# Kernel optimization log

Measured on AMD Instinct MI355X. Metric: run time of the kernel, lower is better.

Reference implementation:

```python
import jax, jax.numpy as jnp
import numpy as np

N, E, F, HID, HEADS, L, OUT = 25000, 400000, 128, 128, 2, 3, 10
C = HID // HEADS
EPS = 1e-5

def _ln(x, g, b):
    m = jnp.mean(x, -1, keepdims=True)
    v = jnp.mean((x - m) ** 2, -1, keepdims=True)
    return (x - m) / jnp.sqrt(v + EPS) * g + b

def _lrelu(x, s=0.01):
    return jnp.where(x >= 0, x, s * x)

def setup_inputs():
    key = jax.random.key(0)
    ks = iter(jax.random.split(key, 80))
    def nrm(shape, fan_in):
        return jax.random.normal(next(ks), shape, dtype=jnp.float32) / np.float32(np.sqrt(fan_in))
    return {
        "x": jax.random.normal(next(ks), (N, F), dtype=jnp.float32),
        "edge_index": jax.random.randint(next(ks), (2, E), 0, N, dtype=jnp.int32),
        "edge_attr": jax.random.uniform(next(ks), (E,), dtype=jnp.float32),
        "task_features": jax.random.normal(next(ks), (4,), dtype=jnp.float32),
        "emb_w": nrm((F, HID), F), "emb_b": jnp.zeros((HID,), jnp.float32),
        "emb_g": jnp.ones((HID,), jnp.float32), "emb_beta": jnp.zeros((HID,), jnp.float32),
        "gat_w": nrm((L, HID, HID), HID),
        "gat_as": nrm((L, HEADS, C), C), "gat_ad": nrm((L, HEADS, C), C),
        "gat_bias": jnp.zeros((L, HID), jnp.float32),
        "ec_w1": nrm((L, 2 * HID, HID), 2 * HID), "ec_b1": jnp.zeros((L, HID), jnp.float32),
        "ec_g1": jnp.ones((L, HID), jnp.float32), "ec_be1": jnp.zeros((L, HID), jnp.float32),
        "ec_w2": nrm((L, HID, HID), HID), "ec_b2": jnp.zeros((L, HID), jnp.float32),
        "ec_g2": jnp.ones((L, HID), jnp.float32), "ec_be2": jnp.zeros((L, HID), jnp.float32),
        "norm_g": jnp.ones((L, HID), jnp.float32), "norm_b": jnp.zeros((L, HID), jnp.float32),
        "task_w": nrm((4, HID), 4), "task_b": jnp.zeros((HID,), jnp.float32),
        "task_g": jnp.ones((HID,), jnp.float32), "task_beta": jnp.zeros((HID,), jnp.float32),
        "pa_w1": nrm((HID, HID // 2), HID), "pa_b1": jnp.zeros((HID // 2,), jnp.float32),
        "pa_w2": nrm((HID // 2, 1), HID // 2), "pa_b2": jnp.zeros((1,), jnp.float32),
        "v_w1": nrm((2 * HID, HID), 2 * HID), "v_b1": jnp.zeros((HID,), jnp.float32),
        "v_g": jnp.ones((HID,), jnp.float32), "v_be": jnp.zeros((HID,), jnp.float32),
        "v_w2": nrm((HID, 1), HID), "v_b2": jnp.zeros((1,), jnp.float32),
        "a_w1": nrm((2 * HID, HID), 2 * HID), "a_b1": jnp.zeros((HID,), jnp.float32),
        "a_g": jnp.ones((HID,), jnp.float32), "a_be": jnp.zeros((HID,), jnp.float32),
        "a_w2": nrm((HID, OUT), HID), "a_b2": jnp.zeros((OUT,), jnp.float32),
    }

def _forward(x, edge_attr, task_features, emb_w, emb_b, emb_g, emb_beta,
             gat_w, gat_as, gat_ad, gat_bias,
             ec_w1, ec_b1, ec_g1, ec_be1, ec_w2, ec_b2, ec_g2, ec_be2,
             norm_g, norm_b, task_w, task_b, task_g, task_beta,
             pa_w1, pa_b1, pa_w2, pa_b2,
             v_w1, v_b1, v_g, v_be, v_w2, v_b2,
             a_w1, a_b1, a_g, a_be, a_w2, a_b2, edge_index):
    src, dst = edge_index[0], edge_index[1]
    loop = jnp.arange(N, dtype=edge_index.dtype)
    src_sl = jnp.concatenate([src, loop])  # PyG GATConv adds self-loops
    dst_sl = jnp.concatenate([dst, loop])
    h = _lrelu(_ln(x @ emb_w + emb_b, emb_g, emb_beta))
    x0 = h
    for i in range(L):
        # --- GATConv (dropout inactive at eval) ---
        ht = (h @ gat_w[i]).reshape(N, HEADS, C)
        a_s = jnp.sum(ht * gat_as[i], -1)  # [N, HEADS]
        a_d = jnp.sum(ht * gat_ad[i], -1)
        e = _lrelu(a_s[src_sl] + a_d[dst_sl], 0.2)  # [E+N, HEADS]
        emax = jax.ops.segment_max(e, dst_sl, num_segments=N)
        ee = jnp.exp(e - emax[dst_sl])
        alpha = ee / jax.ops.segment_sum(ee, dst_sl, num_segments=N)[dst_sl]
        x1 = jax.ops.segment_sum(ht[src_sl] * alpha[:, :, None], dst_sl,
                                 num_segments=N).reshape(N, HID) + gat_bias[i]
        # --- EdgeConv: gather -> MLP -> weighted scatter-add ---
        ef = jnp.concatenate([h[src], h[dst]], axis=1)  # [E, 2*HID]
        ef = _lrelu(_ln(ef @ ec_w1[i] + ec_b1[i], ec_g1[i], ec_be1[i]), 0.2)
        ef = _lrelu(_ln(ef @ ec_w2[i] + ec_b2[i], ec_g2[i], ec_be2[i]), 0.2)
        ef = ef * edge_attr[:, None]
        x2 = jax.ops.segment_sum(ef, dst, num_segments=N)
        h = _lrelu(_ln(x1 + x2, norm_g[i], norm_b[i]))
        if i > 0:
            h = h + x0
            x0 = h
    # attention pooling over all nodes (batch=None path)
    w = jax.nn.softmax((_lrelu(h @ pa_w1 + pa_b1) @ pa_w2 + pa_b2)[:, 0])
    gf = jnp.sum(h * w[:, None], axis=0)  # [HID]
    te = _lrelu(_ln(task_features @ task_w + task_b, task_g, task_beta))
    cf = jnp.concatenate([gf, te], -1)  # [2*HID]
    value = _lrelu(_ln(cf @ v_w1 + v_b1, v_g, v_be)) @ v_w2 + v_b2
    adv = _lrelu(_ln(cf @ a_w1 + a_b1, a_g, a_be)) @ a_w2 + a_b2
    return value + (adv - jnp.mean(adv, -1, keepdims=True))

def reference(x, edge_index, edge_attr, task_features, emb_w, emb_b, emb_g, emb_beta, gat_w, gat_as, gat_ad, gat_bias, ec_w1, ec_b1, ec_g1, ec_be1, ec_w2, ec_b2, ec_g2, ec_be2, norm_g, norm_b, task_w, task_b, task_g, task_beta, pa_w1, pa_b1, pa_w2, pa_b2, v_w1, v_b1, v_g, v_be, v_w2, v_b2, a_w1, a_b1, a_g, a_be, a_w2, a_b2):
    return _forward(x, edge_attr, task_features, emb_w, emb_b, emb_g, emb_beta, gat_w, gat_as, gat_ad, gat_bias, ec_w1, ec_b1, ec_g1, ec_be1, ec_w2, ec_b2, ec_g2, ec_be2, norm_g, norm_b, task_w, task_b, task_g, task_beta, pa_w1, pa_b1, pa_w2, pa_b2, v_w1, v_b1, v_g, v_be, v_w2, v_b2, a_w1, a_b1, a_g, a_be, a_w2, a_b2, edge_index)
```

## Files before the change

kernel.cpp:

```cpp
#include <hip/hip_runtime.h>
#include <math.h>

#define NN 25000
#define EE 400000
#define LL 3
#define LNEPS 1e-5f
#define EB 64

typedef __attribute__((ext_vector_type(8))) short short8;
typedef __attribute__((ext_vector_type(16))) float f32x16;

__device__ __forceinline__ float lrelu(float x, float s) { return fmaxf(x, x * s); }

__device__ __forceinline__ unsigned int pack_bf2(float lo, float hi) {
    unsigned int ul = __float_as_uint(lo), uh = __float_as_uint(hi);
    ul = (ul + 0x7FFFu + ((ul >> 16) & 1u)) >> 16;
    uh = (uh + 0x7FFFu + ((uh >> 16) & 1u)) >> 16;
    return (uh << 16) | (ul & 0xFFFFu);
}

__device__ __forceinline__ void ln_stats128(float v, float* red, float& mean, float& inv) {
    float sm = v, sq = v * v;
#pragma unroll
    for (int m = 32; m >= 1; m >>= 1) { sm += __shfl_xor(sm, m); sq += __shfl_xor(sq, m); }
    __syncthreads();
    if ((threadIdx.x & 63) == 0) { red[(threadIdx.x >> 6) * 2] = sm; red[(threadIdx.x >> 6) * 2 + 1] = sq; }
    __syncthreads();
    sm = red[0] + red[2]; sq = red[1] + red[3];
    mean = sm * (1.f / 128.f);
    float var = sq * (1.f / 128.f) - mean * mean;
    inv = rsqrtf(var + LNEPS);
}

__global__ void k_hist(const int* __restrict__ dst, int* __restrict__ cnt, int ne)
{
    int i = blockIdx.x * 256 + threadIdx.x;
    if (i < ne) atomicAdd(&cnt[dst[i]], 1);
}

__global__ __launch_bounds__(1024) void k_scan(const int* __restrict__ cnt,
                                               int* __restrict__ starts, int n)
{
    __shared__ int tot[1024];
    int t = threadIdx.x;
    const int PER = (n + 1023) >> 10;
    int i0 = t * PER;
    int s = 0;
    for (int k = 0; k < PER; ++k) { int i = i0 + k; s += (i < n) ? cnt[i] : 0; }
    tot[t] = s;
    __syncthreads();
    for (int off = 1; off < 1024; off <<= 1) {
        int x = (t >= off) ? tot[t - off] : 0;
        __syncthreads();
        tot[t] += x;
        __syncthreads();
    }
    int run = (t > 0) ? tot[t - 1] : 0;
    for (int k = 0; k < PER; ++k) {
        int i = i0 + k;
        if (i < n) { starts[i] = run; run += cnt[i]; }
    }
    if (t == 1023) starts[n] = tot[1023];
}

__global__ void k_scatter(const int* __restrict__ src, const int* __restrict__ dst,
                          const float* __restrict__ ea, int* __restrict__ cursor,
                          int* __restrict__ s_src, int* __restrict__ s_dst,
                          float* __restrict__ s_ea, int ne)
{
    int i = blockIdx.x * 256 + threadIdx.x;
    if (i >= ne) return;
    int d = dst[i];
    int pos = atomicAdd(&cursor[d], 1);
    s_src[pos] = src[i];
    s_dst[pos] = d;
    s_ea[pos] = ea[i];
}

__global__ void k_prep(const float* __restrict__ gat_w, const float* __restrict__ ec_w1,
                       const float* __restrict__ ec_w2, const float* __restrict__ emb_w,
                       uint4* __restrict__ wf)
{
    int g = blockIdx.x * 256 + threadIdx.x;
    int m = g >> 11, f = g & 2047;
    const float* srcm;
    if (m < 3) srcm = gat_w + (size_t)m * 16384;
    else if (m < 9) { int t2 = m - 3; srcm = ec_w1 + (size_t)(t2 >> 1) * 32768 + (size_t)(t2 & 1) * 16384; }
    else if (m < 12) srcm = ec_w2 + (size_t)(m - 9) * 16384;
    else srcm = emb_w;
    int l = f & 63, ks = (f >> 6) & 7, nb = f >> 9;
    int k0 = ks * 16 + (l >> 5) * 8, col = nb * 32 + (l & 31);
    const float* wp = srcm + (size_t)k0 * 128 + col;
    uint4 r;
    r.x = pack_bf2(wp[0],   wp[128]);
    r.y = pack_bf2(wp[256], wp[384]);
    r.z = pack_bf2(wp[512], wp[640]);
    r.w = pack_bf2(wp[768], wp[896]);
    wf[g] = r;
}

__global__ __launch_bounds__(256) void k_emb(
    const float* __restrict__ in, const uint4* __restrict__ wfm,
    const float* __restrict__ bias, const float* __restrict__ g,
    const float* __restrict__ be, float* __restrict__ h,
    float* __restrict__ x0, int nrows)
{
    __shared__ __align__(16) unsigned int sA[64 * 64];
    __shared__ __align__(16) unsigned int sW[2048 * 4];
    float* sU = (float*)sW;
    const int tid = threadIdx.x;
    const int r0 = blockIdx.x * 64;
    {
        int row = tid >> 2, q = tid & 3;
        const float* srcp = in + (size_t)(r0 + row) * 128 + q * 32;
        bool ok = (r0 + row) < nrows;
#pragma unroll
        for (int i = 0; i < 8; ++i) {
            float4 v = ok ? *(const float4*)&srcp[i * 4] : make_float4(0.f, 0.f, 0.f, 0.f);
            int cu = (q * 16 + i * 2) ^ ((row & 15) << 2);
            *(uint2*)&sA[row * 64 + cu] = make_uint2(pack_bf2(v.x, v.y), pack_bf2(v.z, v.w));
        }
    }
    {
        uint4* sW4 = (uint4*)sW;
#pragma unroll
        for (int i = 0; i < 8; ++i) sW4[tid + 256 * i] = wfm[tid + 256 * i];
    }
    __syncthreads();
    const int w = tid >> 6, l = tid & 63;
    const int m0 = (w >> 1) * 32, nhalf = (w & 1);
    f32x16 acc0 = {}, acc1 = {};
#pragma unroll
    for (int ks = 0; ks < 8; ++ks) {
        int rw = m0 + (l & 31);
        int cu = (ks * 8 + (l >> 5) * 4) ^ ((rw & 15) << 2);
        short8 a = *(const short8*)&sA[rw * 64 + cu];
        short8 b0 = *(const short8*)&sW[((nhalf * 16 + ks) * 64 + l) * 4];
        short8 b1 = *(const short8*)&sW[(((nhalf * 2 + 1) * 8 + ks) * 64 + l) * 4];
        acc0 = __builtin_amdgcn_mfma_f32_32x32x16_bf16(a, b0, acc0, 0, 0, 0);
        acc1 = __builtin_amdgcn_mfma_f32_32x32x16_bf16(a, b1, acc1, 0, 0, 0);
    }
    __syncthreads();
    {
        int colbase = nhalf * 64 + (l & 31);
        float bb0 = bias[colbase], bb1 = bias[colbase + 32];
#pragma unroll
        for (int r = 0; r < 16; ++r) {
            int rw = m0 + (r & 3) + 8 * (r >> 2) + 4 * (l >> 5);
            sU[rw * 128 + colbase]      = acc0[r] + bb0;
            sU[rw * 128 + colbase + 32] = acc1[r] + bb1;
        }
    }
    __syncthreads();
    float2 gv = *(const float2*)&g[l * 2];
    float2 bv = *(const float2*)&be[l * 2];
    for (int it = 0; it < 16; ++it) {
        int rw = w * 16 + it;
        int grow = r0 + rw;
        if (grow >= nrows) break;
        float2 v = *(const float2*)&sU[rw * 128 + l * 2];
        float sm = v.x + v.y, sq = v.x * v.x + v.y * v.y;
#pragma unroll
        for (int m = 32; m >= 1; m >>= 1) { sm += __shfl_xor(sm, m); sq += __shfl_xor(sq, m); }
        float mean = sm * (1.f / 128.f);
        float var = sq * (1.f / 128.f) - mean * mean;
        float inv = rsqrtf(var + LNEPS);
        float o0 = lrelu((v.x - mean) * inv * gv.x + bv.x, 0.01f);
        float o1 = lrelu((v.y - mean) * inv * gv.y + bv.y, 0.01f);
        unsigned off = (unsigned)grow * 128u + (unsigned)(l * 2);
        *(float2*)&h[off]  = make_float2(o0, o1);
        *(float2*)&x0[off] = make_float2(o0, o1);
    }
}

__global__ __launch_bounds__(256) void k_gemm3(
    const float* __restrict__ in, const uint4* __restrict__ wf,
    int mht, int mA, int mB, const float* __restrict__ bA,
    float* __restrict__ o0, float* __restrict__ o1, float* __restrict__ o2,
    int nrows)
{
    __shared__ __align__(16) unsigned int sA[64 * 64];
    __shared__ __align__(16) unsigned int sW[2048 * 4];
    const int tid = threadIdx.x;
    const int r0 = blockIdx.x * 64;
    {
        int row = tid >> 2, q = tid & 3;
        const float* srcp = in + (size_t)(r0 + row) * 128 + q * 32;
        bool ok = (r0 + row) < nrows;
#pragma unroll
        for (int i = 0; i < 8; ++i) {
            float4 v = ok ? *(const float4*)&srcp[i * 4] : make_float4(0.f, 0.f, 0.f, 0.f);
            unsigned int p0 = pack_bf2(v.x, v.y), p1 = pack_bf2(v.z, v.w);
            int cu = (q * 16 + i * 2) ^ ((row & 15) << 2);
            *(uint2*)&sA[row * 64 + cu] = make_uint2(p0, p1);
        }
    }
    __syncthreads();
    const int w = tid >> 6, l = tid & 63;
    const int m0 = (w >> 1) * 32, nhalf = (w & 1);
    short8 af[8];
#pragma unroll
    for (int ks = 0; ks < 8; ++ks) {
        int row = m0 + (l & 31);
        int cu = (ks * 8 + (l >> 5) * 4) ^ ((row & 15) << 2);
        af[ks] = *(const short8*)&sA[row * 64 + cu];
    }
    auto do_mat = [&](int mat, float* out, const float* bp) {
        __syncthreads();
        {
            const uint4* wsrc = wf + (size_t)mat * 2048;
            uint4* sW4 = (uint4*)sW;
#pragma unroll
            for (int i = 0; i < 8; ++i) sW4[tid + 256 * i] = wsrc[tid + 256 * i];
        }
        __syncthreads();
        f32x16 acc0 = {}, acc1 = {};
        const int nb0 = nhalf * 2;
#pragma unroll
        for (int ks = 0; ks < 8; ++ks) {
            short8 b0 = *(const short8*)&sW[((nb0 * 8 + ks) * 64 + l) * 4];
            short8 b1v = *(const short8*)&sW[(((nb0 + 1) * 8 + ks) * 64 + l) * 4];
            acc0 = __builtin_amdgcn_mfma_f32_32x32x16_bf16(af[ks], b0, acc0, 0, 0, 0);
            acc1 = __builtin_amdgcn_mfma_f32_32x32x16_bf16(af[ks], b1v, acc1, 0, 0, 0);
        }
        int colbase = nhalf * 64 + (l & 31);
        float badd0 = bp ? bp[colbase] : 0.f;
        float badd1 = bp ? bp[colbase + 32] : 0.f;
#pragma unroll
        for (int r = 0; r < 16; ++r) {
            int row = r0 + m0 + (r & 3) + 8 * (r >> 2) + 4 * (l >> 5);
            if (row < nrows) {
                unsigned off = (unsigned)row * 128u + (unsigned)colbase;
                out[off]      = acc0[r] + badd0;
                out[off + 32] = acc1[r] + badd1;
            }
        }
    };
    do_mat(mht, o0, nullptr);
    do_mat(mA, o1, bA);
    do_mat(mB, o2, nullptr);
}

__global__ __launch_bounds__(512) void k_node_scores(
    const float* __restrict__ ht, const float* __restrict__ A, const float* __restrict__ B,
    const float* __restrict__ as_, const float* __restrict__ ad_,
    float* __restrict__ a_s, float* __restrict__ a_d,
    float* __restrict__ denom, float* __restrict__ selfe,
    float* __restrict__ rsA, float* __restrict__ rsB, int n)
{
    int wv = threadIdx.x >> 6, ln = threadIdx.x & 63;
    int node = blockIdx.x * 8 + wv;
    if (node >= n) return;
    unsigned off = (unsigned)node * 128u + (unsigned)(ln * 2);
    float2 hv = *(const float2*)&ht[off];
    float2 av = *(const float2*)&A[off];
    float2 bv = *(const float2*)&B[off];
    float2 wsv = *(const float2*)&as_[ln * 2];
    float2 wdv = *(const float2*)&ad_[ln * 2];
    float ss = hv.x * wsv.x + hv.y * wsv.y;
    float sd = hv.x * wdv.x + hv.y * wdv.y;
    float sa = av.x + av.y, sb = bv.x + bv.y;
#pragma unroll
    for (int m = 16; m >= 1; m >>= 1) {
        ss += __shfl_xor(ss, m); sd += __shfl_xor(sd, m);
        sa += __shfl_xor(sa, m); sb += __shfl_xor(sb, m);
    }
    float sa2 = sa + __shfl_xor(sa, 32);
    float sb2 = sb + __shfl_xor(sb, 32);
    if ((ln & 31) == 0) {
        int hd = ln >> 5;
        a_s[node * 2 + hd] = ss;
        a_d[node * 2 + hd] = sd;
        float ev = expf(lrelu(ss + sd, 0.2f));
        denom[node * 2 + hd] = ev;
        selfe[node * 2 + hd] = ev;
        if (hd == 0) { rsA[node] = sa2; rsB[node] = sb2; }
    }
}

__global__ void k_edge_denom2(const int* __restrict__ s_src, const int* __restrict__ s_dst,
                              const float* __restrict__ a_s, const float* __restrict__ a_d,
                              float* __restrict__ denom, int ne)
{
    int base = (blockIdx.x * 256 + threadIdx.x) * 8;
    if (base >= ne) return;
    int curd = -1;
    float acc0 = 0.f, acc1 = 0.f;
    for (int k = 0; k < 8; ++k) {
        int e = base + k;
        if (e >= ne) break;
        int s = s_src[e], d = s_dst[e];
        float v0 = expf(lrelu(a_s[(unsigned)(s * 2)]     + a_d[(unsigned)(d * 2)],     0.2f));
        float v1 = expf(lrelu(a_s[(unsigned)(s * 2 + 1)] + a_d[(unsigned)(d * 2 + 1)], 0.2f));
        if (d != curd) {
            if (curd >= 0) { atomicAdd(&denom[curd * 2], acc0); atomicAdd(&denom[curd * 2 + 1], acc1); }
            curd = d; acc0 = v0; acc1 = v1;
        } else { acc0 += v0; acc1 += v1; }
    }
    if (curd >= 0) { atomicAdd(&denom[curd * 2], acc0); atomicAdd(&denom[curd * 2 + 1], acc1); }
}

__global__ void k_xsum_init(const float* __restrict__ ht, const float* __restrict__ selfe,
                            const float* __restrict__ denom,
                            const float* __restrict__ gbias, float* __restrict__ xsum, int n)
{
    unsigned idx = blockIdx.x * blockDim.x + threadIdx.x;
    if (idx >= (unsigned)n * 128u) return;
    unsigned node = idx >> 7, c = idx & 127, hd = c >> 6;
    float alpha = selfe[node * 2 + hd] / denom[node * 2 + hd];
    xsum[idx] = gbias[c] + ht[idx] * alpha;
}

__global__ __launch_bounds__(512) void k_edge_main(
    const float* __restrict__ Abuf, const float* __restrict__ Bbuf,
    const float* __restrict__ ht,
    const int* __restrict__ s_src, const int* __restrict__ s_dst,
    const float* __restrict__ s_ea,
    const float* __restrict__ a_s, const float* __restrict__ a_d,
    const float* __restrict__ denom,
    const uint4* __restrict__ w2f,
    const float* __restrict__ rsA, const float* __restrict__ rsB,
    const float* __restrict__ g1, const float* __restrict__ be1,
    const float* __restrict__ b2, const float* __restrict__ g2, const float* __restrict__ be2,
    float* __restrict__ xsum, int ne)
{
    __shared__ __align__(16) unsigned int sWB[2048 * 4];
    __shared__ __align__(16) unsigned int sT32[EB * 64];
    __shared__ int   sS[EB], sD[EB];
    __shared__ float sEA[EB], sM[EB];
    __shared__ float sAl[EB * 2];
    __shared__ float sG1[128], sE1[128], sB2[128], sG2[128], sE2[128];
    float* sU = (float*)sWB;

    const int tid = threadIdx.x;
    {
        uint4* sWB4 = (uint4*)sWB;
#pragma unroll
        for (int i = 0; i < 4; ++i) { int f = tid + 512 * i; sWB4[f] = w2f[f]; }
    }
    if (tid < 128) {
        sG1[tid] = g1[tid]; sE1[tid] = be1[tid];
        sB2[tid] = b2[tid]; sG2[tid] = g2[tid]; sE2[tid] = be2[tid];
    }
    const int e0 = blockIdx.x * EB;
    const int nev = (ne - e0 < EB) ? (ne - e0) : EB;
    if (tid < EB) {
        if (tid < nev) {
            int s = s_src[e0 + tid], d = s_dst[e0 + tid];
            sS[tid] = s; sD[tid] = d; sEA[tid] = s_ea[e0 + tid];
            sM[tid] = (rsA[s] + rsB[d]) * (1.f / 128.f);
        } else { sS[tid] = 0; sD[tid] = -1; sEA[tid] = 0.f; sM[tid] = 0.f; }
    }
    if (tid < 2 * EB) {
        int le = tid >> 1, hd = tid & 1;
        float al = 0.f;
        if (le < nev) {
            int e = e0 + le;
            int s = s_src[e], d = s_dst[e];
            float ev = lrelu(a_s[(unsigned)(s * 2 + hd)] + a_d[(unsigned)(d * 2 + hd)], 0.2f);
            al = expf(ev) / denom[(unsigned)(d * 2 + hd)];
        }
        sAl[le * 2 + hd] = al;
    }
    __syncthreads();

    const int wv = tid >> 6, ln = tid & 63;
    const unsigned ln2 = (unsigned)(ln * 2);
    {
        const float g1a = sG1[ln * 2], g1b = sG1[ln * 2 + 1];
        const float e1a = sE1[ln * 2], e1b = sE1[ln * 2 + 1];
        for (int j = 0; j < 8; ++j) {
            int e = wv * 8 + j;
            if (e < nev) {
                unsigned s = (unsigned)sS[e], d = (unsigned)sD[e];
                float mean = sM[e];
                float2 av = *(const float2*)&Abuf[s * 128u + ln2];
                float2 bv = *(const float2*)&Bbuf[d * 128u + ln2];
                float v0 = av.x + bv.x - mean;
                float v1 = av.y + bv.y - mean;
                float sq = v0 * v0 + v1 * v1;
#pragma unroll
                for (int m = 32; m >= 1; m >>= 1) sq += __shfl_xor(sq, m);
                float inv = rsqrtf(sq * (1.f / 128.f) + LNEPS);
                float t0 = lrelu(v0 * inv * g1a + e1a, 0.2f);
                float t1 = lrelu(v1 * inv * g1b + e1b, 0.2f);
                sT32[e * 64 + (ln ^ ((e & 15) << 2))] = pack_bf2(t0, t1);
            }
        }
    }
    __syncthreads();

    {
        const int w = wv, l = ln;
        const int m0 = (w >> 2) * 32, n0 = (w & 3) * 32;
        f32x16 acc = {};
#pragma unroll
        for (int ks = 0; ks < 8; ++ks) {
            int row = m0 + (l & 31);
            int colu = (ks * 8 + (l >> 5) * 4) ^ ((row & 15) << 2);
            short8 a = *(const short8*)&sT32[row * 64 + colu];
            short8 b = *(const short8*)&sWB[((((w & 3) * 8 + ks) * 64 + l)) * 4];
            acc = __builtin_amdgcn_mfma_f32_32x32x16_bf16(a, b, acc, 0, 0, 0);
        }
        __syncthreads();
        float b2c = sB2[n0 + (l & 31)];
#pragma unroll
        for (int r = 0; r < 16; ++r) {
            int row = m0 + (r & 3) + 8 * (r >> 2) + 4 * (l >> 5);
            sU[row * 128 + n0 + (l & 31)] = acc[r] + b2c;
        }
    }
    __syncthreads();

    {
        const float g2a = sG2[ln * 2], g2b = sG2[ln * 2 + 1];
        const float e2a = sE2[ln * 2], e2b = sE2[ln * 2 + 1];
        int curd = -1;
        float acc0 = 0.f, acc1 = 0.f;
        for (int j = 0; j < 8; ++j) {
            int e = wv * 8 + j;
            if (e >= nev) break;
            unsigned s = (unsigned)sS[e];
            int d = sD[e];
            float2 uv = *(const float2*)&sU[e * 128 + ln * 2];
            float u0 = uv.x, u1 = uv.y;
            float sm = u0 + u1, sq = u0 * u0 + u1 * u1;
#pragma unroll
            for (int m = 32; m >= 1; m >>= 1) { sm += __shfl_xor(sm, m); sq += __shfl_xor(sq, m); }
            float mean = sm * (1.f / 128.f);
            float var = sq * (1.f / 128.f) - mean * mean;
            float inv = rsqrtf(var + LNEPS);
            float eav = sEA[e];
            float v0 = lrelu((u0 - mean) * inv * g2a + e2a, 0.2f) * eav;
            float v1 = lrelu((u1 - mean) * inv * g2b + e2b, 0.2f) * eav;
            float al = sAl[e * 2 + (ln >> 5)];
            float2 hv = *(const float2*)&ht[s * 128u + ln2];
            v0 += hv.x * al;
            v1 += hv.y * al;
            if (d != curd) {
                if (curd >= 0) {
                    atomicAdd(&xsum[(unsigned)curd * 128u + ln2], acc0);
                    atomicAdd(&xsum[(unsigned)curd * 128u + ln2 + 1], acc1);
                }
                curd = d; acc0 = v0; acc1 = v1;
            } else { acc0 += v0; acc1 += v1; }
        }
        if (curd >= 0) {
            atomicAdd(&xsum[(unsigned)curd * 128u + ln2], acc0);
            atomicAdd(&xsum[(unsigned)curd * 128u + ln2 + 1], acc1);
        }
    }
}

__global__ __launch_bounds__(512) void k_norm8(const float* __restrict__ xsum,
                                               const float* __restrict__ g,
                                               const float* __restrict__ b,
                                               float* __restrict__ x0,
                                               float* __restrict__ h, int n, int layer)
{
    int wv = threadIdx.x >> 6, ln = threadIdx.x & 63;
    int node = blockIdx.x * 8 + wv;
    if (node >= n) return;
    unsigned off = (unsigned)node * 128u + (unsigned)(ln * 2);
    float2 v = *(const float2*)&xsum[off];
    float sm = v.x + v.y, sq = v.x * v.x + v.y * v.y;
#pragma unroll
    for (int m = 32; m >= 1; m >>= 1) { sm += __shfl_xor(sm, m); sq += __shfl_xor(sq, m); }
    float mean = sm * (1.f / 128.f);
    float var = sq * (1.f / 128.f) - mean * mean;
    float inv = rsqrtf(var + LNEPS);
    float2 gv = *(const float2*)&g[ln * 2];
    float2 bv = *(const float2*)&b[ln * 2];
    float val0 = lrelu((v.x - mean) * inv * gv.x + bv.x, 0.01f);
    float val1 = lrelu((v.y - mean) * inv * gv.y + bv.y, 0.01f);
    if (layer > 0) {
        float2 x0v = *(const float2*)&x0[off];
        val0 += x0v.x; val1 += x0v.y;
        *(float2*)&x0[off] = make_float2(val0, val1);
    }
    *(float2*)&h[off] = make_float2(val0, val1);
}

__global__ __launch_bounds__(256) void k_pool_score(const float* __restrict__ h,
    const float* __restrict__ w1, const float* __restrict__ b1,
    const float* __restrict__ w2, const float* __restrict__ b2,
    float* __restrict__ score, int n)
{
    int wv = threadIdx.x >> 6, ln = threadIdx.x & 63;
    int node = blockIdx.x * 4 + wv;
    if (node >= n) return;
    float acc = b1[ln];
    const float* hr = h + (size_t)node * 128;
    for (int k = 0; k < 128; ++k) acc += hr[k] * w1[k * 64 + ln];
    acc = lrelu(acc, 0.01f) * w2[ln];
#pragma unroll
    for (int m = 32; m >= 1; m >>= 1) acc += __shfl_xor(acc, m);
    if (ln == 0) score[node] = acc + b2[0];
}

__global__ __launch_bounds__(256) void k_softmax_reduce(const float* __restrict__ score,
                                                        float* __restrict__ stats,
                                                        float* __restrict__ gf, int n)
{
    __shared__ float red[8];
    int t = threadIdx.x;
    float mx = -1e30f;
    for (int i = t; i < n; i += 256) mx = fmaxf(mx, score[i]);
#pragma unroll
    for (int m = 32; m >= 1; m >>= 1) mx = fmaxf(mx, __shfl_xor(mx, m));
    if ((t & 63) == 0) red[t >> 6] = mx;
    __syncthreads();
    mx = fmaxf(fmaxf(red[0], red[1]), fmaxf(red[2], red[3]));
    float s = 0.f;
    for (int i = t; i < n; i += 256) s += expf(score[i] - mx);
#pragma unroll
    for (int m = 32; m >= 1; m >>= 1) s += __shfl_xor(s, m);
    if ((t & 63) == 0) red[4 + (t >> 6)] = s;
    __syncthreads();
    s = red[4] + red[5] + red[6] + red[7];
    if (t == 0) { stats[0] = mx; stats[1] = s; }
    if (t < 128) gf[t] = 0.f;
}

__global__ __launch_bounds__(128) void k_gf(const float* __restrict__ h,
                                            const float* __restrict__ score,
                                            const float* __restrict__ stats,
                                            float* __restrict__ gf, int n)
{
    int c = threadIdx.x;
    float mx = stats[0], invZ = 1.f / stats[1];
    int per = (n + gridDim.x - 1) / gridDim.x;
    int n0 = blockIdx.x * per;
    int n1 = n0 + per; if (n1 > n) n1 = n;
    float acc = 0.f;
    for (int i = n0; i < n1; ++i)
        acc += expf(score[i] - mx) * invZ * h[(size_t)i * 128 + c];
    atomicAdd(&gf[c], acc);
}

__global__ __launch_bounds__(128) void k_head(
    const float* __restrict__ gf, const float* __restrict__ tf,
    const float* __restrict__ task_w, const float* __restrict__ task_b,
    const float* __restrict__ task_g, const float* __restrict__ task_be,
    const float* __restrict__ v_w1, const float* __restrict__ v_b1,
    const float* __restrict__ v_g, const float* __restrict__ v_be,
    const float* __restrict__ v_w2, const float* __restrict__ v_b2,
    const float* __restrict__ a_w1, const float* __restrict__ a_b1,
    const float* __restrict__ a_g, const float* __restrict__ a_be,
    const float* __restrict__ a_w2, const float* __restrict__ a_b2,
    float* __restrict__ out)
{
    __shared__ float cf[256], hbuf[128], red[4], sc[2], adv[10];
    int t = threadIdx.x;
    float mean, inv;
    float te = task_b[t];
#pragma unroll
    for (int k = 0; k < 4; ++k) te += tf[k] * task_w[k * 128 + t];
    ln_stats128(te, red, mean, inv);
    te = lrelu((te - mean) * inv * task_g[t] + task_be[t], 0.01f);
    cf[t] = gf[t]; cf[128 + t] = te;
    __syncthreads();
    float v = v_b1[t];
    for (int k = 0; k < 256; ++k) v += cf[k] * v_w1[k * 128 + t];
    ln_stats128(v, red, mean, inv);
    v = lrelu((v - mean) * inv * v_g[t] + v_be[t], 0.01f);
    float pv = v * v_w2[t];
#pragma unroll
    for (int m = 32; m >= 1; m >>= 1) pv += __shfl_xor(pv, m);
    __syncthreads();
    if ((t & 63) == 0) red[t >> 6] = pv;
    __syncthreads();
    if (t == 0) sc[0] = red[0] + red[1] + v_b2[0];
    float a = a_b1[t];
    for (int k = 0; k < 256; ++k) a += cf[k] * a_w1[k * 128 + t];
    ln_stats128(a, red, mean, inv);
    a = lrelu((a - mean) * inv * a_g[t] + a_be[t], 0.01f);
    hbuf[t] = a;
    __syncthreads();
    if (t < 10) {
        float s = a_b2[t];
        for (int c = 0; c < 128; ++c) s += hbuf[c] * a_w2[c * 10 + t];
        adv[t] = s;
    }
    __syncthreads();
    if (t == 0) {
        float m10 = 0.f;
        for (int o = 0; o < 10; ++o) m10 += adv[o];
        sc[1] = m10 * 0.1f;
    }
    __syncthreads();
    if (t < 10) out[t] = sc[0] + adv[t] - sc[1];
}

extern "C" void kernel_launch(void* const* d_in, const int* in_sizes, int n_in,
                              void* d_out, int out_size, void* d_ws, size_t ws_size,
                              hipStream_t stream)
{
    const float* x        = (const float*)d_in[0];
    const int*   ei       = (const int*)d_in[1];
    const float* ea       = (const float*)d_in[2];
    const float* tf       = (const float*)d_in[3];
    const float* emb_w    = (const float*)d_in[4];
    const float* emb_b    = (const float*)d_in[5];
    const float* emb_g    = (const float*)d_in[6];
    const float* emb_beta = (const float*)d_in[7];
    const float* gat_w    = (const float*)d_in[8];
    const float* gat_as   = (const float*)d_in[9];
    const float* gat_ad   = (const float*)d_in[10];
    const float* gat_bias = (const float*)d_in[11];
    const float* ec_w1    = (const float*)d_in[12];
    const float* ec_b1    = (const float*)d_in[13];
    const float* ec_g1    = (const float*)d_in[14];
    const float* ec_be1   = (const float*)d_in[15];
    const float* ec_w2    = (const float*)d_in[16];
    const float* ec_b2    = (const float*)d_in[17];
    const float* ec_g2    = (const float*)d_in[18];
    const float* ec_be2   = (const float*)d_in[19];
    const float* norm_g   = (const float*)d_in[20];
    const float* norm_b   = (const float*)d_in[21];
    const float* task_w   = (const float*)d_in[22];
    const float* task_b   = (const float*)d_in[23];
    const float* task_g   = (const float*)d_in[24];
    const float* task_be  = (const float*)d_in[25];
    const float* pa_w1    = (const float*)d_in[26];
    const float* pa_b1    = (const float*)d_in[27];
    const float* pa_w2    = (const float*)d_in[28];
    const float* pa_b2    = (const float*)d_in[29];
    const float* v_w1     = (const float*)d_in[30];
    const float* v_b1     = (const float*)d_in[31];
    const float* v_g      = (const float*)d_in[32];
    const float* v_be     = (const float*)d_in[33];
    const float* v_w2     = (const float*)d_in[34];
    const float* v_b2     = (const float*)d_in[35];
    const float* a_w1     = (const float*)d_in[36];
    const float* a_b1     = (const float*)d_in[37];
    const float* a_g      = (const float*)d_in[38];
    const float* a_be     = (const float*)d_in[39];
    const float* a_w2     = (const float*)d_in[40];
    const float* a_b2     = (const float*)d_in[41];

    const int n = in_sizes[0] / 128;
    const int e = in_sizes[2];
    const int* src = ei;
    const int* dst = ei + e;

    float* ws = (float*)d_ws;
    uint4* wf = (uint4*)ws;
    float* base = ws + 13 * 2048 * 4;
    const size_t NR = (size_t)n * 128;
    float* h    = base;
    float* x0   = base + NR;
    float* ht   = base + 2 * NR;
    float* A    = base + 3 * NR;
    float* B    = base + 4 * NR;
    float* xs   = base + 5 * NR;
    float* a_s  = base + 6 * NR;
    float* a_d  = a_s + (size_t)n * 2;
    float* den  = a_d + (size_t)n * 2;
    float* selfe = den + (size_t)n * 2;
    float* rsA  = selfe + (size_t)n * 2;
    float* rsB  = rsA + n;
    float* score = rsB + n;
    float* stats = score + n;
    float* gf    = stats + 2;
    int*   cnt    = (int*)(gf + 128);
    int*   starts = cnt + n;
    int*   s_src  = starts + (n + 1);
    int*   s_dst  = s_src + e;
    float* s_ea   = (float*)(s_dst + e);

    const int ng64 = (n + 63) / 64;
    const int ng8 = (n + 7) / 8;

    hipMemsetAsync(cnt, 0, (size_t)n * sizeof(int), stream);
    k_hist<<<(e + 255) / 256, 256, 0, stream>>>(dst, cnt, e);
    k_scan<<<1, 1024, 0, stream>>>(cnt, starts, n);
    hipMemcpyAsync(cnt, starts, (size_t)n * sizeof(int), hipMemcpyDeviceToDevice, stream);
    k_scatter<<<(e + 255) / 256, 256, 0, stream>>>(src, dst, ea, cnt, s_src, s_dst, s_ea, e);
    k_prep<<<104, 256, 0, stream>>>(gat_w, ec_w1, ec_w2, emb_w, wf);

    k_emb<<<ng64, 256, 0, stream>>>(x, wf + (size_t)12 * 2048, emb_b, emb_g, emb_beta, h, x0, n);

    for (int i = 0; i < LL; ++i) {
        k_gemm3<<<ng64, 256, 0, stream>>>(h, wf, i, 3 + 2 * i, 4 + 2 * i,
                                          ec_b1 + i * 128, ht, A, B, n);
        k_node_scores<<<ng8, 512, 0, stream>>>(ht, A, B, gat_as + i * 128, gat_ad + i * 128,
                                               a_s, a_d, den, selfe, rsA, rsB, n);
        k_edge_denom2<<<((e + 7) / 8 + 255) / 256, 256, 0, stream>>>(s_src, s_dst, a_s, a_d, den, e);
        k_xsum_init<<<(n * 128 + 255) / 256, 256, 0, stream>>>(ht, selfe, den,
                                                               gat_bias + i * 128, xs, n);
        k_edge_main<<<(e + EB - 1) / EB, 512, 0, stream>>>(A, B, ht, s_src, s_dst, s_ea,
                                                           a_s, a_d, den,
                                                           wf + (size_t)(9 + i) * 2048,
                                                           rsA, rsB,
                                                           ec_g1 + i * 128, ec_be1 + i * 128,
                                                           ec_b2 + i * 128, ec_g2 + i * 128, ec_be2 + i * 128,
                                                           xs, e);
        k_norm8<<<ng8, 512, 0, stream>>>(xs, norm_g + i * 128, norm_b + i * 128, x0, h, n, i);
    }

    k_pool_score<<<(n + 3) / 4, 256, 0, stream>>>(h, pa_w1, pa_b1, pa_w2, pa_b2, score, n);
    k_softmax_reduce<<<1, 256, 0, stream>>>(score, stats, gf, n);
    k_gf<<<200, 128, 0, stream>>>(h, score, stats, gf, n);
    k_head<<<1, 128, 0, stream>>>(gf, tf, task_w, task_b, task_g, task_be,
                                  v_w1, v_b1, v_g, v_be, v_w2, v_b2,
                                  a_w1, a_b1, a_g, a_be, a_w2, a_b2,
                                  (float*)d_out);
}
```

Before: 803.5 us.

## Store GEMM outputs ht, A, B as packed bf16 to halve gather traffic

```diff
diff --git a/kernel.cpp b/kernel.cpp
--- a/kernel.cpp
+++ b/kernel.cpp
@@ -18,6 +18,8 @@
     uh = (uh + 0x7FFFu + ((uh >> 16) & 1u)) >> 16;
     return (uh << 16) | (ul & 0xFFFFu);
 }
+__device__ __forceinline__ float bf_lo(unsigned int u) { return __uint_as_float(u << 16); }
+__device__ __forceinline__ float bf_hi(unsigned int u) { return __uint_as_float(u & 0xFFFF0000u); }
 
 __device__ __forceinline__ void ln_stats128(float v, float* red, float& mean, float& inv) {
     float sm = v, sq = v * v;
@@ -176,7 +178,7 @@
 __global__ __launch_bounds__(256) void k_gemm3(
     const float* __restrict__ in, const uint4* __restrict__ wf,
     int mht, int mA, int mB, const float* __restrict__ bA,
-    float* __restrict__ o0, float* __restrict__ o1, float* __restrict__ o2,
+    unsigned* __restrict__ o0, unsigned* __restrict__ o1, unsigned* __restrict__ o2,
     int nrows)
 {
     __shared__ __align__(16) unsigned int sA[64 * 64];
@@ -205,7 +207,10 @@
         int cu = (ks * 8 + (l >> 5) * 4) ^ ((row & 15) << 2);
         af[ks] = *(const short8*)&sA[row * 64 + cu];
     }
-    auto do_mat = [&](int mat, float* out, const float* bp) {
+    const int c = l & 31;
+    const bool evenl = (c & 1) == 0;
+    const unsigned uidx = (unsigned)(nhalf * 32 + (evenl ? (c >> 1) : (16 + (c >> 1))));
+    auto do_mat = [&](int mat, unsigned* out, const float* bp) {
         __syncthreads();
         {
             const uint4* wsrc = wf + (size_t)mat * 2048;
@@ -223,16 +228,19 @@
             acc0 = __builtin_amdgcn_mfma_f32_32x32x16_bf16(af[ks], b0, acc0, 0, 0, 0);
             acc1 = __builtin_amdgcn_mfma_f32_32x32x16_bf16(af[ks], b1v, acc1, 0, 0, 0);
         }
-        int colbase = nhalf * 64 + (l & 31);
+        int colbase = nhalf * 64 + c;
         float badd0 = bp ? bp[colbase] : 0.f;
         float badd1 = bp ? bp[colbase + 32] : 0.f;
 #pragma unroll
         for (int r = 0; r < 16; ++r) {
+            float v0 = acc0[r] + badd0;
+            float v1 = acc1[r] + badd1;
+            float v0p = __shfl_xor(v0, 1);
+            float v1p = __shfl_xor(v1, 1);
             int row = r0 + m0 + (r & 3) + 8 * (r >> 2) + 4 * (l >> 5);
             if (row < nrows) {
-                unsigned off = (unsigned)row * 128u + (unsigned)colbase;
-                out[off]      = acc0[r] + badd0;
-                out[off + 32] = acc1[r] + badd1;
+                unsigned val = evenl ? pack_bf2(v0, v0p) : pack_bf2(v1p, v1);
+                out[(unsigned)row * 64u + uidx] = val;
             }
         }
     };
@@ -242,7 +250,8 @@
 }
 
 __global__ __launch_bounds__(512) void k_node_scores(
-    const float* __restrict__ ht, const float* __restrict__ A, const float* __restrict__ B,
+    const unsigned* __restrict__ htp, const unsigned* __restrict__ Apk,
+    const unsigned* __restrict__ Bpk,
     const float* __restrict__ as_, const float* __restrict__ ad_,
     float* __restrict__ a_s, float* __restrict__ a_d,
     float* __restrict__ denom, float* __restrict__ selfe,
@@ -251,15 +260,14 @@
     int wv = threadIdx.x >> 6, ln = threadIdx.x & 63;
     int node = blockIdx.x * 8 + wv;
     if (node >= n) return;
-    unsigned off = (unsigned)node * 128u + (unsigned)(ln * 2);
-    float2 hv = *(const float2*)&ht[off];
-    float2 av = *(const float2*)&A[off];
-    float2 bv = *(const float2*)&B[off];
+    unsigned off = (unsigned)node * 64u + (unsigned)ln;
+    unsigned hv = htp[off], av = Apk[off], bv = Bpk[off];
+    float h0 = bf_lo(hv), h1 = bf_hi(hv);
     float2 wsv = *(const float2*)&as_[ln * 2];
     float2 wdv = *(const float2*)&ad_[ln * 2];
-    float ss = hv.x * wsv.x + hv.y * wsv.y;
-    float sd = hv.x * wdv.x + hv.y * wdv.y;
-    float sa = av.x + av.y, sb = bv.x + bv.y;
+    float ss = h0 * wsv.x + h1 * wsv.y;
+    float sd = h0 * wdv.x + h1 * wdv.y;
+    float sa = bf_lo(av) + bf_hi(av), sb = bf_lo(bv) + bf_hi(bv);
 #pragma unroll
     for (int m = 16; m >= 1; m >>= 1) {
         ss += __shfl_xor(ss, m); sd += __shfl_xor(sd, m);
@@ -300,20 +308,24 @@
     if (curd >= 0) { atomicAdd(&denom[curd * 2], acc0); atomicAdd(&denom[curd * 2 + 1], acc1); }
 }
 
-__global__ void k_xsum_init(const float* __restrict__ ht, const float* __restrict__ selfe,
+__global__ void k_xsum_init(const unsigned* __restrict__ htp, const float* __restrict__ selfe,
                             const float* __restrict__ denom,
                             const float* __restrict__ gbias, float* __restrict__ xsum, int n)
 {
     unsigned idx = blockIdx.x * blockDim.x + threadIdx.x;
-    if (idx >= (unsigned)n * 128u) return;
-    unsigned node = idx >> 7, c = idx & 127, hd = c >> 6;
+    if (idx >= (unsigned)n * 64u) return;
+    unsigned node = idx >> 6, u = idx & 63, hd = u >> 5;
     float alpha = selfe[node * 2 + hd] / denom[node * 2 + hd];
-    xsum[idx] = gbias[c] + ht[idx] * alpha;
+    unsigned hv = htp[idx];
+    float2 o;
+    o.x = gbias[u * 2]     + bf_lo(hv) * alpha;
+    o.y = gbias[u * 2 + 1] + bf_hi(hv) * alpha;
+    *(float2*)&xsum[node * 128u + u * 2u] = o;
 }
 
 __global__ __launch_bounds__(512) void k_edge_main(
-    const float* __restrict__ Abuf, const float* __restrict__ Bbuf,
-    const float* __restrict__ ht,
+    const unsigned* __restrict__ Apk, const unsigned* __restrict__ Bpk,
+    const unsigned* __restrict__ htp,
     const int* __restrict__ s_src, const int* __restrict__ s_dst,
     const float* __restrict__ s_ea,
     const float* __restrict__ a_s, const float* __restrict__ a_d,
@@ -365,7 +377,6 @@
     __syncthreads();
 
     const int wv = tid >> 6, ln = tid & 63;
-    const unsigned ln2 = (unsigned)(ln * 2);
     {
         const float g1a = sG1[ln * 2], g1b = sG1[ln * 2 + 1];
         const float e1a = sE1[ln * 2], e1b = sE1[ln * 2 + 1];
@@ -374,10 +385,10 @@
             if (e < nev) {
                 unsigned s = (unsigned)sS[e], d = (unsigned)sD[e];
                 float mean = sM[e];
-                float2 av = *(const float2*)&Abuf[s * 128u + ln2];
-                float2 bv = *(const float2*)&Bbuf[d * 128u + ln2];
-                float v0 = av.x + bv.x - mean;
-                float v1 = av.y + bv.y - mean;
+                unsigned av = Apk[s * 64u + ln];
+                unsigned bv = Bpk[d * 64u + ln];
+                float v0 = bf_lo(av) + bf_lo(bv) - mean;
+                float v1 = bf_hi(av) + bf_hi(bv) - mean;
                 float sq = v0 * v0 + v1 * v1;
 #pragma unroll
                 for (int m = 32; m >= 1; m >>= 1) sq += __shfl_xor(sq, m);
@@ -413,6 +424,7 @@
     __syncthreads();
 
     {
+        const unsigned ln2 = (unsigned)(ln * 2);
         const float g2a = sG2[ln * 2], g2b = sG2[ln * 2 + 1];
         const float e2a = sE2[ln * 2], e2b = sE2[ln * 2 + 1];
         int curd = -1;
@@ -434,9 +446,9 @@
             float v0 = lrelu((u0 - mean) * inv * g2a + e2a, 0.2f) * eav;
             float v1 = lrelu((u1 - mean) * inv * g2b + e2b, 0.2f) * eav;
             float al = sAl[e * 2 + (ln >> 5)];
-            float2 hv = *(const float2*)&ht[s * 128u + ln2];
-            v0 += hv.x * al;
-            v1 += hv.y * al;
+            unsigned hv = htp[s * 64u + ln];
+            v0 += bf_lo(hv) * al;
+            v1 += bf_hi(hv) * al;
             if (d != curd) {
                 if (curd >= 0) {
                     atomicAdd(&xsum[(unsigned)curd * 128u + ln2], acc0);
@@ -648,13 +660,14 @@
     uint4* wf = (uint4*)ws;
     float* base = ws + 13 * 2048 * 4;
     const size_t NR = (size_t)n * 128;
+    const size_t NP = (size_t)n * 64;
     float* h    = base;
     float* x0   = base + NR;
-    float* ht   = base + 2 * NR;
-    float* A    = base + 3 * NR;
-    float* B    = base + 4 * NR;
-    float* xs   = base + 5 * NR;
-    float* a_s  = base + 6 * NR;
+    float* xs   = base + 2 * NR;
+    unsigned* htp = (unsigned*)(base + 3 * NR);
+    unsigned* Apk = htp + NP;
+    unsigned* Bpk = Apk + NP;
+    float* a_s  = (float*)(Bpk + NP);
     float* a_d  = a_s + (size_t)n * 2;
     float* den  = a_d + (size_t)n * 2;
     float* selfe = den + (size_t)n * 2;
@@ -683,13 +696,13 @@
 
     for (int i = 0; i < LL; ++i) {
         k_gemm3<<<ng64, 256, 0, stream>>>(h, wf, i, 3 + 2 * i, 4 + 2 * i,
-                                          ec_b1 + i * 128, ht, A, B, n);
-        k_node_scores<<<ng8, 512, 0, stream>>>(ht, A, B, gat_as + i * 128, gat_ad + i * 128,
+                                          ec_b1 + i * 128, htp, Apk, Bpk, n);
+        k_node_scores<<<ng8, 512, 0, stream>>>(htp, Apk, Bpk, gat_as + i * 128, gat_ad + i * 128,
                                                a_s, a_d, den, selfe, rsA, rsB, n);
         k_edge_denom2<<<((e + 7) / 8 + 255) / 256, 256, 0, stream>>>(s_src, s_dst, a_s, a_d, den, e);
-        k_xsum_init<<<(n * 128 + 255) / 256, 256, 0, stream>>>(ht, selfe, den,
-                                                               gat_bias + i * 128, xs, n);
-        k_edge_main<<<(e + EB - 1) / EB, 512, 0, stream>>>(A, B, ht, s_src, s_dst, s_ea,
+        k_xsum_init<<<(n * 64 + 255) / 256, 256, 0, stream>>>(htp, selfe, den,
+                                                              gat_bias + i * 128, xs, n);
+        k_edge_main<<<(e + EB - 1) / EB, 512, 0, stream>>>(Apk, Bpk, htp, s_src, s_dst, s_ea,
                                                            a_s, a_d, den,
                                                            wf + (size_t)(9 + i) * 2048,
                                                            rsA, rsB,
```

Result: no change. 798.1 us (-0.7%).
